# Kernel tuning notes

Hardware: AMD Instinct MI355X
Metric: run time of the kernel (lower is better)

Reference implementation:

```python
import jax, jax.numpy as jnp
import numpy as np

BASE_RES = 0.2
RES_FACTOR = (1.0 - BASE_RES) * 0.9
N_ATOMS = 1024
LATENT = 128
WINDOW = 512
HOP = WINDOW // 2
RES_SAMPLES = 32768
N_FRAMES = RES_SAMPLES // HOP  # 128


def setup_inputs() -> dict:
    key = jax.random.key(0)
    ks = jax.random.split(key, 6)
    x = jax.random.normal(ks[0], (16, 64, LATENT), dtype=jnp.float32)
    W_sel = jax.random.normal(ks[1], (N_ATOMS, LATENT), dtype=jnp.float32) * 0.1
    b_sel = jnp.zeros((N_ATOMS,), dtype=jnp.float32)
    W_mom = jax.random.normal(ks[2], (N_FRAMES, LATENT), dtype=jnp.float32) * 0.1
    b_mom = jnp.zeros((N_FRAMES,), dtype=jnp.float32)
    atoms = jax.random.normal(ks[3], (N_ATOMS, RES_SAMPLES), dtype=jnp.float32) * 0.01
    return {"x": x, "W_sel": W_sel, "b_sel": b_sel, "W_mom": W_mom, "b_mom": b_mom, "atoms": atoms}


def _hann_periodic(n):
    # torch.hann_window default (periodic=True)
    return 0.5 * (1.0 - jnp.cos(2.0 * jnp.pi * jnp.arange(n) / n))


def reference(x, W_sel, b_sel, W_mom, b_mom, atoms):
    # momentum: sigmoid -> affine -> log-cumsum-exp decay per frame
    mom = BASE_RES + jax.nn.sigmoid(jnp.einsum('bel,fl->bef', x, W_mom) + b_mom) * RES_FACTOR
    mom = jnp.exp(jnp.cumsum(jnp.log(1e-12 + mom), axis=-1))  # (B,E,F)

    # softmax atom selection and mixing
    sel = jax.nn.softmax(jnp.einsum('bel,al->bea', x, W_sel) + b_sel, axis=-1)
    res = jnp.einsum('bea,as->bes', sel, atoms)  # (B,E,S)

    # windowed_audio: pad by hop, unfold, apply hann window
    padded = jnp.pad(res, ((0, 0), (0, 0), (0, HOP)))
    idx = jnp.arange(N_FRAMES)[:, None] * HOP + jnp.arange(WINDOW)[None, :]
    frames = padded[..., idx] * _hann_periodic(WINDOW)  # (B,E,F,W)

    # per-frame unit norm, then momentum scaling
    norm = jnp.linalg.norm(frames, axis=-1, keepdims=True)
    frames = frames / (norm + 1e-8)
    frames = frames * mom[..., None]

    # overlap-add with hop = WINDOW//2 (no extra window)
    B, E = frames.shape[0], frames.shape[1]
    first = frames[..., :HOP].reshape(B, E, -1)
    second = frames[..., HOP:].reshape(B, E, -1)
    out = jnp.pad(first, ((0, 0), (0, 0), (0, HOP))) + jnp.pad(second, ((0, 0), (0, 0), (HOP, 0)))
    return out[..., :RES_SAMPLES], mom
```

## Files before the change

kernel.cpp:

```cpp
#include <hip/hip_runtime.h>


typedef __attribute__((ext_vector_type(8))) short short8;
typedef __attribute__((ext_vector_type(4))) float f32x4;

typedef __attribute__((address_space(1))) void GV;
typedef __attribute__((address_space(3))) void LV;

__device__ __forceinline__ unsigned short f2bf(float f) {
    union { float f; unsigned u; } c; c.f = f;
    unsigned u = c.u;
    u = (u + 0x7FFFu + ((u >> 16) & 1u)) >> 16;
    return (unsigned short)u;
}
__device__ __forceinline__ float bf2f(unsigned short h) {
    union { unsigned u; float f; } c; c.u = ((unsigned)h) << 16; return c.f;
}

__global__ __launch_bounds__(256) void k_convert(
        const float* __restrict__ x, const float* __restrict__ Wsel,
        const float* __restrict__ Wmom,
        unsigned short* __restrict__ xbf, unsigned short* __restrict__ wbf,
        float* __restrict__ WmomT) {
    const int i = (blockIdx.x * 256 + threadIdx.x) * 4;
    {
        float4 v = *(const float4*)(x + i);
        uint2 q;
        q.x = (unsigned)f2bf(v.x) | ((unsigned)f2bf(v.y) << 16);
        q.y = (unsigned)f2bf(v.z) | ((unsigned)f2bf(v.w) << 16);
        *(uint2*)(xbf + i) = q;
    }
    {
        float4 v = *(const float4*)(Wsel + i);
        uint2 q;
        q.x = (unsigned)f2bf(v.x) | ((unsigned)f2bf(v.y) << 16);
        q.y = (unsigned)f2bf(v.z) | ((unsigned)f2bf(v.w) << 16);
        *(uint2*)(wbf + i) = q;
    }
    if (blockIdx.x < 8) {
        const int f  = blockIdx.x * 16 + (threadIdx.x >> 4);
        const int kc = (threadIdx.x & 15) * 8;
        float4 a = *(const float4*)(Wmom + (size_t)f * 128 + kc);
        float4 b = *(const float4*)(Wmom + (size_t)f * 128 + kc + 4);
        WmomT[(kc + 0) * 128 + f] = a.x; WmomT[(kc + 1) * 128 + f] = a.y;
        WmomT[(kc + 2) * 128 + f] = a.z; WmomT[(kc + 3) * 128 + f] = a.w;
        WmomT[(kc + 4) * 128 + f] = b.x; WmomT[(kc + 5) * 128 + f] = b.y;
        WmomT[(kc + 6) * 128 + f] = b.z; WmomT[(kc + 7) * 128 + f] = b.w;
    }
}

__global__ __launch_bounds__(256) void k_head_gemm(
        const unsigned short* __restrict__ A, const unsigned short* __restrict__ Bm,
        float* __restrict__ logits) {
    __shared__ __align__(16) unsigned short lA[128 * 32];
    __shared__ __align__(16) unsigned short lB[128 * 32];
    const int tid = threadIdx.x;
    const int wave = tid >> 6;
    const int lane = tid & 63;
    const int l15 = lane & 15, quad = lane >> 4;
    const int i0 = blockIdx.x * 128;
    const int j0 = blockIdx.y * 128;
    const int wi = wave >> 1, wj = wave & 1;
    const int rsel = lane >> 2;
    const int koff = (lane & 3) * 8;

    f32x4 acc[4][4] = {};

    for (int kt = 0; kt < 4; ++kt) {
        const int kbase = kt * 32;
#pragma unroll
        for (int c = 0; c < 2; ++c) {
            const int row = c * 64 + wave * 16 + rsel;
            const unsigned short* ga = A + (size_t)(i0 + row) * 128 + kbase + koff;
            const unsigned short* gb = Bm + (size_t)(j0 + row) * 128 + kbase + koff;
            unsigned short* la = lA + (c * 64 + wave * 16) * 32;
            unsigned short* lb = lB + (c * 64 + wave * 16) * 32;
            __builtin_amdgcn_global_load_lds((GV*)ga, (LV*)la, 16, 0, 0);
            __builtin_amdgcn_global_load_lds((GV*)gb, (LV*)lb, 16, 0, 0);
        }
        __syncthreads();

        short8 af[4], bf[4];
#pragma unroll
        for (int ti = 0; ti < 4; ++ti)
            af[ti] = *(const short8*)(lA + (wi * 64 + ti * 16 + l15) * 32 + quad * 8);
#pragma unroll
        for (int tj = 0; tj < 4; ++tj)
            bf[tj] = *(const short8*)(lB + (wj * 64 + tj * 16 + l15) * 32 + quad * 8);
#pragma unroll
        for (int ti = 0; ti < 4; ++ti)
#pragma unroll
            for (int tj = 0; tj < 4; ++tj)
                acc[ti][tj] = __builtin_amdgcn_mfma_f32_16x16x32_bf16(
                    af[ti], bf[tj], acc[ti][tj], 0, 0, 0);
        __syncthreads();
    }

#pragma unroll
    for (int ti = 0; ti < 4; ++ti) {
#pragma unroll
        for (int tj = 0; tj < 4; ++tj) {
            const int mrow = j0 + wj * 64 + tj * 16 + l15;
            const int abase = i0 + wi * 64 + ti * 16 + quad * 4;
            f32x4 v = acc[ti][tj];
            float4 o; o.x = v[0]; o.y = v[1]; o.z = v[2]; o.w = v[3];
            *(float4*)(logits + (size_t)mrow * 1024 + abase) = o;
        }
    }
}

__global__ __launch_bounds__(256) void k_softmax_mom(
        const float* __restrict__ logits_g, const float* __restrict__ bsel,
        const float* __restrict__ x, const float* __restrict__ WmomT,
        const float* __restrict__ bmom, unsigned short* __restrict__ sel,
        float* __restrict__ momout) {
    __shared__ float xs[128];
    __shared__ float logits[1024];
    __shared__ float mvals[128];
    __shared__ float wred[4];
    __shared__ float sstat[2];
    const int tid = threadIdx.x;
    const int m = blockIdx.x;

    if (tid < 32) *(float4*)&xs[tid * 4] = *(const float4*)(x + (size_t)m * 128 + tid * 4);
    for (int a = tid; a < 1024; a += 256)
        logits[a] = logits_g[(size_t)m * 1024 + a] + bsel[a];
    __syncthreads();

    if (tid < 128) {
        float acc = bmom[tid];
#pragma unroll 8
        for (int k = 0; k < 128; ++k)
            acc += xs[k] * WmomT[k * 128 + tid];
        float sig = 1.f / (1.f + __expf(-acc));
        mvals[tid] = 0.2f + sig * 0.72f;
    }

    float mx = -1e30f;
    for (int a = tid; a < 1024; a += 256) mx = fmaxf(mx, logits[a]);
#pragma unroll
    for (int off = 32; off; off >>= 1) mx = fmaxf(mx, __shfl_xor(mx, off, 64));
    if ((tid & 63) == 0) wred[tid >> 6] = mx;
    __syncthreads();
    if (tid == 0) sstat[0] = fmaxf(fmaxf(wred[0], wred[1]), fmaxf(wred[2], wred[3]));
    __syncthreads();
    mx = sstat[0];

    float psum = 0.f;
    for (int a = tid; a < 1024; a += 256) {
        float e = __expf(logits[a] - mx);
        logits[a] = e;
        psum += e;
    }
#pragma unroll
    for (int off = 32; off; off >>= 1) psum += __shfl_xor(psum, off, 64);
    if ((tid & 63) == 0) wred[tid >> 6] = psum;
    __syncthreads();
    if (tid == 0) sstat[1] = wred[0] + wred[1] + wred[2] + wred[3];
    __syncthreads();
    const float inv = 1.f / sstat[1];
    for (int a = tid; a < 1024; a += 256)
        sel[(size_t)m * 1024 + a] = f2bf(logits[a] * inv);

    if (tid == 0) {
        float p = 1.f;
        for (int f = 0; f < 128; ++f) {
            p *= (mvals[f] + 1e-12f);
            momout[(size_t)m * 128 + f] = p;
        }
    }
}

__global__ __launch_bounds__(256) void k_transpose(
        const float* __restrict__ atoms, unsigned short* __restrict__ atomsT) {
    __shared__ float t[64][65];
    const int tid = threadIdx.x;
    const int s0 = blockIdx.x * 64;
    const int a0 = blockIdx.y * 64;

    {
        const int r0 = tid >> 4;
        const int c4 = (tid & 15) * 4;
        for (int rr = r0; rr < 64; rr += 16) {
            float4 v = *(const float4*)(atoms + (size_t)(a0 + rr) * 32768 + s0 + c4);
            t[rr][c4] = v.x; t[rr][c4 + 1] = v.y; t[rr][c4 + 2] = v.z; t[rr][c4 + 3] = v.w;
        }
    }
    __syncthreads();
    {
        const int sl = tid >> 2;
        const int seg = (tid & 3) * 16;
        unsigned short* dst = atomsT + (size_t)(s0 + sl) * 1024 + a0 + seg;
        unsigned pk[8];
#pragma unroll
        for (int i = 0; i < 16; i += 2) {
            unsigned short h0 = f2bf(t[seg + i][sl]);
            unsigned short h1 = f2bf(t[seg + i + 1][sl]);
            pk[i >> 1] = (unsigned)h0 | ((unsigned)h1 << 16);
        }
        uint4 q0; q0.x = pk[0]; q0.y = pk[1]; q0.z = pk[2]; q0.w = pk[3];
        uint4 q1; q1.x = pk[4]; q1.y = pk[5]; q1.z = pk[6]; q1.w = pk[7];
        *(uint4*)(dst) = q0;
        *(uint4*)(dst + 8) = q1;
    }
}

__global__ __launch_bounds__(256) void k_gemm(
        const unsigned short* __restrict__ A, const unsigned short* __restrict__ Bm,
        unsigned short* __restrict__ res) {
    __shared__ __align__(16) unsigned short buf[17408];
    unsigned short* lA = buf;
    unsigned short* lB = buf + 4096;
    const int tid = threadIdx.x;
    const int wave = tid >> 6;
    const int lane = tid & 63;
    const int l15 = lane & 15, quad = lane >> 4;
    const int bid = blockIdx.x;
    const int s_tile = ((bid >> 6) << 3) | (bid & 7);
    const int m_tile = (bid >> 3) & 7;
    const int j0 = m_tile * 128;
    const int i0 = s_tile * 128;
    const int wi = wave >> 1, wj = wave & 1;
    const int rsel = lane >> 2;
    const int koff = (lane & 3) * 8;

    f32x4 acc[4][4] = {};

    for (int kt = 0; kt < 32; ++kt) {
        const int kbase = kt * 32;
#pragma unroll
        for (int c = 0; c < 2; ++c) {
            const int row = c * 64 + wave * 16 + rsel;
            const unsigned short* ga = A + (size_t)(i0 + row) * 1024 + kbase + koff;
            const unsigned short* gb = Bm + (size_t)(j0 + row) * 1024 + kbase + koff;
            unsigned short* la = lA + (c * 64 + wave * 16) * 32;
            unsigned short* lb = lB + (c * 64 + wave * 16) * 32;
            __builtin_amdgcn_global_load_lds((GV*)ga, (LV*)la, 16, 0, 0);
            __builtin_amdgcn_global_load_lds((GV*)gb, (LV*)lb, 16, 0, 0);
        }
        __syncthreads();

        short8 af[4], bf[4];
#pragma unroll
        for (int ti = 0; ti < 4; ++ti)
            af[ti] = *(const short8*)(lA + (wi * 64 + ti * 16 + l15) * 32 + quad * 8);
#pragma unroll
        for (int tj = 0; tj < 4; ++tj)
            bf[tj] = *(const short8*)(lB + (wj * 64 + tj * 16 + l15) * 32 + quad * 8);
#pragma unroll
        for (int ti = 0; ti < 4; ++ti)
#pragma unroll
            for (int tj = 0; tj < 4; ++tj)
                acc[ti][tj] = __builtin_amdgcn_mfma_f32_16x16x32_bf16(
                    af[ti], bf[tj], acc[ti][tj], 0, 0, 0);
        __syncthreads();
    }

#pragma unroll
    for (int ti = 0; ti < 4; ++ti) {
#pragma unroll
        for (int tj = 0; tj < 4; ++tj) {
            const int mloc = wj * 64 + tj * 16 + l15;
            const int sloc = wi * 64 + ti * 16 + quad * 4;
            f32x4 v = acc[ti][tj];
            uint2 q;
            q.x = (unsigned)f2bf(v[0]) | ((unsigned)f2bf(v[1]) << 16);
            q.y = (unsigned)f2bf(v[2]) | ((unsigned)f2bf(v[3]) << 16);
            *(uint2*)(buf + mloc * 136 + sloc) = q;
        }
    }
    __syncthreads();
    {
        const int r = tid >> 1;
        const int h = tid & 1;
        unsigned short* grow = res + (size_t)(j0 + r) * 32768 + i0 + h * 64;
        const unsigned short* lrow = buf + r * 136 + h * 64;
#pragma unroll
        for (int j = 0; j < 8; ++j)
            *(uint4*)(grow + j * 8) = *(const uint4*)(lrow + j * 8);
    }
}

__global__ __launch_bounds__(256) void k_final(
        const unsigned short* __restrict__ res, const float* __restrict__ mom,
        float* __restrict__ out) {
    __shared__ float hann[512];
    __shared__ float P0[128];
    __shared__ float P1[128];
    __shared__ float scl[129];
    const int tid = threadIdx.x;
    const int m = blockIdx.x;
    const unsigned short* row = res + (size_t)m * 32768;

    hann[tid]       = 0.5f * (1.f - cosf(6.283185307179586f * (float)tid / 512.f));
    hann[tid + 256] = 0.5f * (1.f - cosf(6.283185307179586f * (float)(tid + 256) / 512.f));
    if (tid == 0) scl[0] = 0.f;
    __syncthreads();

    const int wave = tid >> 6, lane = tid & 63;
    const int ih = (lane & 31) * 8;
    for (int cp = wave; cp < 64; cp += 4) {
        const unsigned short* p = row + cp * 512 + lane * 8;
        uint4 q = *(const uint4*)p;
        float s0 = 0.f, s1 = 0.f;
        const unsigned w[4] = {q.x, q.y, q.z, q.w};
#pragma unroll
        for (int j = 0; j < 4; ++j) {
            float v0 = bf2f((unsigned short)w[j]);
            float v1 = bf2f((unsigned short)(w[j] >> 16));
            float a0 = v0 * hann[ih + j * 2],       a1 = v1 * hann[ih + j * 2 + 1];
            float b0 = v0 * hann[256 + ih + j * 2], b1 = v1 * hann[256 + ih + j * 2 + 1];
            s0 += a0 * a0 + a1 * a1;
            s1 += b0 * b0 + b1 * b1;
        }
#pragma unroll
        for (int off = 1; off <= 16; off <<= 1) {
            s0 += __shfl_xor(s0, off, 64);
            s1 += __shfl_xor(s1, off, 64);
        }
        if ((lane & 31) == 0) {
            const int c = 2 * cp + (lane >> 5);
            P0[c] = s0; P1[c] = s1;
        }
    }
    __syncthreads();
    if (tid < 128) {
        const float n2 = P0[tid] + ((tid < 127) ? P1[tid + 1] : 0.f);
        scl[tid + 1] = mom[(size_t)m * 128 + tid] / (sqrtf(n2) + 1e-8f);
    }
    __syncthreads();

#pragma unroll 4
    for (int j = 0; j < 32; ++j) {
        const int s0 = j * 1024 + tid * 4;
        const int f1 = s0 >> 8, i1 = s0 & 255;
        const float sc1 = scl[f1 + 1];
        const float sc0 = scl[f1];
        uint2 rp = *(const uint2*)(row + s0);
        float4 o;
        o.x = bf2f((unsigned short)rp.x)         * (hann[i1]     * sc1 + hann[i1 + 256] * sc0);
        o.y = bf2f((unsigned short)(rp.x >> 16)) * (hann[i1 + 1] * sc1 + hann[i1 + 257] * sc0);
        o.z = bf2f((unsigned short)rp.y)         * (hann[i1 + 2] * sc1 + hann[i1 + 258] * sc0);
        o.w = bf2f((unsigned short)(rp.y >> 16)) * (hann[i1 + 3] * sc1 + hann[i1 + 259] * sc0);
        *(float4*)(out + (size_t)m * 32768 + s0) = o;
    }
}

extern "C" void kernel_launch(void* const* d_in, const int* in_sizes, int n_in,
                              void* d_out, int out_size, void* d_ws, size_t ws_size,
                              hipStream_t stream) {
    const float* x     = (const float*)d_in[0];
    const float* Wsel  = (const float*)d_in[1];
    const float* bsel  = (const float*)d_in[2];
    const float* Wmom  = (const float*)d_in[3];
    const float* bmom  = (const float*)d_in[4];
    const float* atoms = (const float*)d_in[5];

    float* out    = (float*)d_out;
    float* momout = out + (size_t)1024 * 32768;

    unsigned char* ws = (unsigned char*)d_ws;
    unsigned short* atomsT = (unsigned short*)(ws);
    unsigned short* sel    = (unsigned short*)(ws + 67108864);
    unsigned short* res    = (unsigned short*)(ws + 69206016);
    float*          logits = (float*)res;
    unsigned short* xbf    = (unsigned short*)(ws + 69206016 + 4194304);
    unsigned short* wbf    = (unsigned short*)(ws + 69206016 + 4194304 + 262144);
    float*          WmomT  = (float*)(ws + 69206016 + 4194304 + 524288);

    k_convert<<<128, 256, 0, stream>>>(x, Wsel, Wmom, xbf, wbf, WmomT);
    k_head_gemm<<<dim3(8, 8), 256, 0, stream>>>(wbf, xbf, logits);
    k_softmax_mom<<<1024, 256, 0, stream>>>(logits, bsel, x, WmomT, bmom, sel, momout);
    k_transpose<<<dim3(512, 16), 256, 0, stream>>>(atoms, atomsT);
    k_gemm<<<2048, 256, 0, stream>>>(atomsT, sel, res);
    k_final<<<1024, 256, 0, stream>>>(res, momout, out);
}
```

Measured before the change: 402.6 us.

## Rewrite atom-mix GEMM with 256x256 tiles and 4-stage LDS pipeline

Rewrites the main bf16 MFMA GEMM so each 512-thread block computes a 256x256 output tile instead of 128x128. Operands stream into a 4-deep ring of LDS buffers via global_load_lds, with explicit vmcnt waits so loads for tile t+3 overlap MFMAs on tile t. LDS layouts are XOR-swizzled to avoid bank conflicts, the block index is remapped across XCDs, and s_setprio is raised around the MFMA burst. The goal is to cut per-iteration barrier stalls and raise operand reuse. In exchange it uses 128KB of LDS per block, which limits occupancy to one block per CU, and register pressure is higher.

```diff
diff --git a/kernel.cpp b/kernel.cpp
--- a/kernel.cpp
+++ b/kernel.cpp
@@ -205,79 +205,116 @@
     }
 }
 
-__global__ __launch_bounds__(256) void k_gemm(
+__global__ __launch_bounds__(512, 2) void k_gemm(
         const unsigned short* __restrict__ A, const unsigned short* __restrict__ Bm,
         unsigned short* __restrict__ res) {
-    __shared__ __align__(16) unsigned short buf[17408];
-    unsigned short* lA = buf;
-    unsigned short* lB = buf + 4096;
+    __shared__ __align__(16) unsigned short smem[65536];
     const int tid = threadIdx.x;
+    const int lane = tid & 63;
     const int wave = tid >> 6;
-    const int lane = tid & 63;
     const int l15 = lane & 15, quad = lane >> 4;
-    const int bid = blockIdx.x;
-    const int s_tile = ((bid >> 6) << 3) | (bid & 7);
-    const int m_tile = (bid >> 3) & 7;
-    const int j0 = m_tile * 128;
-    const int i0 = s_tile * 128;
-    const int wi = wave >> 1, wj = wave & 1;
-    const int rsel = lane >> 2;
-    const int koff = (lane & 3) * 8;
-
-    f32x4 acc[4][4] = {};
-
-    for (int kt = 0; kt < 32; ++kt) {
-        const int kbase = kt * 32;
-#pragma unroll
-        for (int c = 0; c < 2; ++c) {
-            const int row = c * 64 + wave * 16 + rsel;
-            const unsigned short* ga = A + (size_t)(i0 + row) * 1024 + kbase + koff;
-            const unsigned short* gb = Bm + (size_t)(j0 + row) * 1024 + kbase + koff;
-            unsigned short* la = lA + (c * 64 + wave * 16) * 32;
-            unsigned short* lb = lB + (c * 64 + wave * 16) * 32;
-            __builtin_amdgcn_global_load_lds((GV*)ga, (LV*)la, 16, 0, 0);
-            __builtin_amdgcn_global_load_lds((GV*)gb, (LV*)lb, 16, 0, 0);
-        }
-        __syncthreads();
-
-        short8 af[4], bf[4];
-#pragma unroll
-        for (int ti = 0; ti < 4; ++ti)
-            af[ti] = *(const short8*)(lA + (wi * 64 + ti * 16 + l15) * 32 + quad * 8);
-#pragma unroll
-        for (int tj = 0; tj < 4; ++tj)
-            bf[tj] = *(const short8*)(lB + (wj * 64 + tj * 16 + l15) * 32 + quad * 8);
-#pragma unroll
-        for (int ti = 0; ti < 4; ++ti)
-#pragma unroll
-            for (int tj = 0; tj < 4; ++tj)
-                acc[ti][tj] = __builtin_amdgcn_mfma_f32_16x16x32_bf16(
-                    af[ti], bf[tj], acc[ti][tj], 0, 0, 0);
-        __syncthreads();
-    }
-
-#pragma unroll
-    for (int ti = 0; ti < 4; ++ti) {
+    const int wm = wave >> 2;
+    const int wn = wave & 3;
+
+    const int wg = ((blockIdx.x & 7) << 6) | (blockIdx.x >> 3);
+    const int m_tile = wg & 3;
+    const int s_tile = wg >> 2;
+    const int i0 = s_tile << 8;
+    const int j0 = m_tile << 8;
+
+    const unsigned short* gA[2];
+    const unsigned short* gB[2];
+    int st_ld[2];
+#pragma unroll
+    for (int r = 0; r < 2; ++r) {
+        const int qq = r * 64 + (tid >> 3);
+        const int Gs = (tid & 7) ^ (qq & 7);
+        const int row = 2 * qq + (Gs >> 2);
+        const int g8 = (Gs & 3) * 8;
+        st_ld[r] = r * 4096 + tid * 8;
+        gA[r] = A  + (size_t)(i0 + row) * 1024 + g8;
+        gB[r] = Bm + (size_t)(j0 + row) * 1024 + g8;
+    }
+
+    const int Gp = (((l15 & 1) << 2) | quad) ^ (l15 >> 1);
+    const int aoff = wm * 4096 + (l15 >> 1) * 64 + Gp * 8;
+    const int boff = wn * 2048 + (l15 >> 1) * 64 + Gp * 8;
+
+#define STAGE(T) {                                                            \
+    unsigned short* bb = smem + ((T) & 3) * 16384;                            \
+    const int kb = (T) * 32;                                                  \
+    __builtin_amdgcn_global_load_lds((GV*)(gA[0] + kb), (LV*)(bb + st_ld[0]), 16, 0, 0); \
+    __builtin_amdgcn_global_load_lds((GV*)(gA[1] + kb), (LV*)(bb + st_ld[1]), 16, 0, 0); \
+    __builtin_amdgcn_global_load_lds((GV*)(gB[0] + kb), (LV*)(bb + 8192 + st_ld[0]), 16, 0, 0); \
+    __builtin_amdgcn_global_load_lds((GV*)(gB[1] + kb), (LV*)(bb + 8192 + st_ld[1]), 16, 0, 0); }
+
+#define TILE(T, VMC, DOSTAGE) {                                               \
+    asm volatile("s_waitcnt vmcnt(" VMC ")" ::: "memory");                    \
+    __builtin_amdgcn_s_barrier();                                             \
+    if (DOSTAGE) STAGE((T) + 3);                                              \
+    const unsigned short* bufA = smem + ((T) & 3) * 16384;                    \
+    const unsigned short* bufB = bufA + 8192;                                 \
+    short8 a8[8], b8[4];                                                      \
+    _Pragma("unroll")                                                         \
+    for (int tj = 0; tj < 4; ++tj)                                            \
+        b8[tj] = *(const short8*)(bufB + boff + tj * 512);                    \
+    _Pragma("unroll")                                                         \
+    for (int ti = 0; ti < 8; ++ti)                                            \
+        a8[ti] = *(const short8*)(bufA + aoff + ti * 512);                    \
+    __builtin_amdgcn_s_setprio(1);                                            \
+    _Pragma("unroll")                                                         \
+    for (int ti = 0; ti < 8; ++ti)                                            \
+    _Pragma("unroll")                                                         \
+    for (int tj = 0; tj < 4; ++tj)                                            \
+        acc[ti][tj] = __builtin_amdgcn_mfma_f32_16x16x32_bf16(                \
+            a8[ti], b8[tj], acc[ti][tj], 0, 0, 0);                            \
+    __builtin_amdgcn_s_setprio(0); }
+
+    f32x4 acc[8][4] = {};
+
+    STAGE(0); STAGE(1); STAGE(2);
+    for (int t = 0; t < 29; ++t)
+        TILE(t, "8", true);
+    TILE(29, "8", false);
+    TILE(30, "4", false);
+    TILE(31, "0", false);
+
+#undef TILE
+#undef STAGE
+
+    asm volatile("s_waitcnt lgkmcnt(0)" ::: "memory");
+    __builtin_amdgcn_s_barrier();
+#pragma unroll
+    for (int ti = 0; ti < 8; ++ti) {
 #pragma unroll
         for (int tj = 0; tj < 4; ++tj) {
-            const int mloc = wj * 64 + tj * 16 + l15;
-            const int sloc = wi * 64 + ti * 16 + quad * 4;
+            const int mloc = wn * 64 + tj * 16 + l15;
+            const int g = wm * 32 + ti * 4 + quad;
+            const int gs = g ^ (mloc & 15);
             f32x4 v = acc[ti][tj];
-            uint2 q;
-            q.x = (unsigned)f2bf(v[0]) | ((unsigned)f2bf(v[1]) << 16);
-            q.y = (unsigned)f2bf(v[2]) | ((unsigned)f2bf(v[3]) << 16);
-            *(uint2*)(buf + mloc * 136 + sloc) = q;
-        }
-    }
-    __syncthreads();
+            uint2 q2;
+            q2.x = (unsigned)f2bf(v[0]) | ((unsigned)f2bf(v[1]) << 16);
+            q2.y = (unsigned)f2bf(v[2]) | ((unsigned)f2bf(v[3]) << 16);
+            *(uint2*)(smem + mloc * 256 + gs * 4) = q2;
+        }
+    }
+    asm volatile("s_waitcnt lgkmcnt(0)" ::: "memory");
+    __builtin_amdgcn_s_barrier();
     {
         const int r = tid >> 1;
         const int h = tid & 1;
-        unsigned short* grow = res + (size_t)(j0 + r) * 32768 + i0 + h * 64;
-        const unsigned short* lrow = buf + r * 136 + h * 64;
-#pragma unroll
-        for (int j = 0; j < 8; ++j)
-            *(uint4*)(grow + j * 8) = *(const uint4*)(lrow + j * 8);
+        unsigned short* grow = res + (size_t)(j0 + r) * 32768 + i0 + h * 128;
+        const unsigned short* lrow = smem + r * 256;
+        const int rx = r & 15;
+#pragma unroll
+        for (int j = 0; j < 32; j += 2) {
+            const int g0 = (h * 32 + j) ^ rx;
+            const int g1 = (h * 32 + j + 1) ^ rx;
+            uint2 u0 = *(const uint2*)(lrow + g0 * 4);
+            uint2 u1 = *(const uint2*)(lrow + g1 * 4);
+            uint4 q; q.x = u0.x; q.y = u0.y; q.z = u1.x; q.w = u1.y;
+            *(uint4*)(grow + j * 4) = q;
+        }
     }
 }
 
@@ -372,6 +409,6 @@
     k_head_gemm<<<dim3(8, 8), 256, 0, stream>>>(wbf, xbf, logits);
     k_softmax_mom<<<1024, 256, 0, stream>>>(logits, bsel, x, WmomT, bmom, sel, momout);
     k_transpose<<<dim3(512, 16), 256, 0, stream>>>(atoms, atomsT);
-    k_gemm<<<2048, 256, 0, stream>>>(atomsT, sel, res);
+    k_gemm<<<512, 512, 0, stream>>>(atomsT, sel, res);
     k_final<<<1024, 256, 0, stream>>>(res, momout, out);
 }
```

Result: faster. 387.7 us (-3.7%).
